# Kernel optimization log

Measured on AMD Instinct MI355X. Metric: run time of the kernel, lower is better.

The kernel has to match this reference:

```python
import jax, jax.numpy as jnp
import numpy as np


def _ln(x, g, b, eps=1e-5):
    m = jnp.mean(x, axis=-1, keepdims=True)
    v = jnp.var(x, axis=-1, keepdims=True)
    return (x - m) * jax.lax.rsqrt(v + eps) * g + b


def setup_inputs() -> dict:
    key = jax.random.key(0)
    ks = jax.random.split(key, 24)
    B, Cin, Cout, Rout, N1, N2 = 8, 256, 512, 256, 4096, 1024
    s = 0.02
    f32 = jnp.float32
    return {
        "l1": jax.random.normal(ks[0], (B, Cin, N1), f32),
        "xyz1": jax.random.normal(ks[1], (B, 3, N1), f32),
        "l2": jax.random.normal(ks[2], (B, Cout, N2), f32),
        "xyz2": jax.random.normal(ks[3], (B, 3, N2), f32),
        # im_choose 1x1 convs (no bias)
        "q1_w": jax.random.normal(ks[4], (Cout, Cin), f32) * s,
        "k1_w": jax.random.normal(ks[5], (Cout, Cin), f32) * s,
        # mlp: Linear(Cin,Cin) -> LN(Cin) -> ReLU -> Linear(Cin,Cout)
        "mlp_w1": jax.random.normal(ks[6], (Cin, Cin), f32) * s,
        "mlp_b1": jnp.zeros((Cin,), f32),
        "mlp_g1": jnp.ones((Cin,), f32),
        "mlp_be1": jnp.zeros((Cin,), f32),
        "mlp_w2": jax.random.normal(ks[7], (Cout, Cin), f32) * s,
        "mlp_b2": jnp.zeros((Cout,), f32),
        # slefAttention 1x1 convs (no bias); pos1 conv is unused in forward
        "qw": jax.random.normal(ks[8], (Cout, Cout), f32) * s,
        "kw": jax.random.normal(ks[9], (Cout, Cout), f32) * s,
        "vw": jax.random.normal(ks[10], (Cout, Cout), f32) * s,
        "posw": jax.random.normal(ks[11], (Cout, 3), f32) * s,
        # IMFF.norm LayerNorm(Cout)
        "norm_g": jnp.ones((Cout,), f32),
        "norm_b": jnp.zeros((Cout,), f32),
        # mlp1: Linear(Cout,Cout) -> LN(Cout) -> ReLU -> Linear(Cout,Rout)
        "m1_w1": jax.random.normal(ks[12], (Cout, Cout), f32) * s,
        "m1_b1": jnp.zeros((Cout,), f32),
        "m1_g": jnp.ones((Cout,), f32),
        "m1_be": jnp.zeros((Cout,), f32),
        "m1_w2": jax.random.normal(ks[13], (Rout, Cout), f32) * s,
        "m1_b2": jnp.zeros((Rout,), f32),
    }


def reference(l1, xyz1, l2, xyz2, q1_w, k1_w, mlp_w1, mlp_b1, mlp_g1, mlp_be1,
              mlp_w2, mlp_b2, qw, kw, vw, posw, norm_g, norm_b,
              m1_w1, m1_b1, m1_g, m1_be, m1_w2, m1_b2):
    Cout = q1_w.shape[0]
    top_k = l2.shape[2]
    scale = jnp.sqrt(jnp.float32(Cout))

    # ---- im_choose: top-k selection of source points via attention row 0 ----
    q1 = jnp.einsum('oc,bcn->bon', q1_w, l1)          # [B,Cout,N1]
    k1 = jnp.einsum('oc,bcn->bon', k1_w, l1)          # [B,Cout,N1]
    e1 = jnp.einsum('bcn,bcm->bnm', q1, k1) / scale   # [B,N1,N1]
    att1 = jax.nn.softmax(e1, axis=-1)
    att_se = att1[:, 0, :]                            # [B,N1]
    _, idx = jax.lax.top_k(att_se, top_k)             # [B,K]
    l1_sel = jnp.take_along_axis(l1, idx[:, None, :], axis=-1)    # [B,Cin,K]
    p1_sel = jnp.take_along_axis(xyz1, idx[:, None, :], axis=-1)  # [B,3,K]

    # ---- mlp on gathered features ----
    h = jnp.swapaxes(l1_sel, 1, 2)                    # [B,K,Cin]
    h = jax.nn.relu(_ln(h @ mlp_w1.T + mlp_b1, mlp_g1, mlp_be1))
    h = h @ mlp_w2.T + mlp_b2                         # [B,K,Cout]
    x2 = jnp.swapaxes(h, 1, 2)                        # [B,Cout,K]

    # ---- slefAttention (cross): x1=l2/xyz2 queries, x2/p1_sel keys+values ----
    pos_q = jnp.einsum('oc,bcn->bon', posw, xyz2)     # [B,Cout,N2]
    pos_k = jnp.einsum('oc,bcn->bon', posw, p1_sel)   # [B,Cout,K]
    q = jnp.einsum('oc,bcn->bon', qw, l2 + pos_q)
    k = jnp.einsum('oc,bcn->bon', kw, x2 + pos_k)
    v = jnp.einsum('oc,bcn->bon', vw, x2)
    e = jnp.einsum('bcn,bcm->bnm', q, k) / scale      # [B,N2,K]
    att = jax.nn.softmax(e, axis=-1)
    o = jnp.einsum('bnm,bcm->bcn', att, v) + l2       # [B,Cout,N2]
    o = jnp.swapaxes(o, 1, 2)                         # [B,N2,Cout]

    # ---- norm + leaky_relu + mlp1 head ----
    o = jax.nn.leaky_relu(_ln(o, norm_g, norm_b), 0.01)
    o = jax.nn.relu(_ln(o @ m1_w1.T + m1_b1, m1_g, m1_be))
    o = o @ m1_w2.T + m1_b2                           # [B,N2,Rout]
    return jnp.swapaxes(o, 1, 2)                      # [B,Rout,N2]
```

## Files before the change

### kernel.cpp

```cpp
#include <hip/hip_runtime.h>
#include <math.h>


typedef __attribute__((ext_vector_type(8))) short short8x;
typedef __attribute__((ext_vector_type(4))) float f32x4;

__device__ __forceinline__ unsigned short f2b(float f) {
  unsigned int u = __float_as_uint(f);
  unsigned int r = u + 0x7FFFu + ((u >> 16) & 1u);
  return (unsigned short)(r >> 16);
}
__device__ __forceinline__ float b2f(unsigned short h) {
  return __uint_as_float(((unsigned int)h) << 16);
}

__device__ __forceinline__ void cp16(const unsigned short* g, unsigned short* l) {
  __builtin_amdgcn_global_load_lds(
      (const __attribute__((address_space(1))) void*)g,
      (__attribute__((address_space(3))) void*)l, 16, 0, 0);
}

__global__ void __launch_bounds__(256) sel_qw_kernel(
    const float* __restrict__ l1, const float* __restrict__ q1w,
    const float* __restrict__ k1w, float* __restrict__ wvec) {
  const int b = blockIdx.x;
  const int t = threadIdx.x;
  __shared__ float col[256];
  __shared__ float q1v[512];
  col[t] = l1[(long)b * 256 * 4096 + (long)t * 4096];
  __syncthreads();
  for (int o = t; o < 512; o += 256) {
    float s = 0.f;
    const float* row = q1w + (long)o * 256;
    for (int c = 0; c < 256; ++c) s += row[c] * col[c];
    q1v[o] = s;
  }
  __syncthreads();
  float s = 0.f;
  for (int o = 0; o < 512; ++o) s += k1w[(long)o * 256 + t] * q1v[o];
  wvec[b * 256 + t] = s;
}

__global__ void __launch_bounds__(256) sel_scores_kernel(
    const float* __restrict__ l1, const float* __restrict__ wvec,
    float* __restrict__ scores) {
  const int b = blockIdx.y;
  const int m = blockIdx.x * 256 + threadIdx.x;
  __shared__ float w[256];
  w[threadIdx.x] = wvec[b * 256 + threadIdx.x];
  __syncthreads();
  const float* base = l1 + (long)b * 256 * 4096 + m;
  float s = 0.f;
  for (int c = 0; c < 256; ++c) s += w[c] * base[(long)c * 4096];
  scores[b * 4096 + m] = s;
}

__global__ void __launch_bounds__(256) topk_select_kernel(
    const float* __restrict__ scores, int* __restrict__ idx_out) {
  const int b = blockIdx.x;
  const int t = threadIdx.x;
  __shared__ unsigned int keys[4096];
  __shared__ unsigned int hist[256];
  __shared__ unsigned int sc_prefix, sc_krem;
  __shared__ int s_bin;
  __shared__ unsigned int partial_gt[256], partial_eq[256];

  for (int m = t; m < 4096; m += 256) {
    unsigned int u = __float_as_uint(scores[b * 4096 + m]);
    u ^= (u & 0x80000000u) ? 0xFFFFFFFFu : 0x80000000u;
    keys[m] = u;
  }
  if (t == 0) { sc_prefix = 0u; sc_krem = 1024u; }
  __syncthreads();

  unsigned int prefmask = 0u;
  for (int shift = 24; shift >= 0; shift -= 8) {
    hist[t] = 0u;
    if (t == 0) s_bin = 0;
    __syncthreads();
    const unsigned int prefix = sc_prefix;
    for (int m = t; m < 4096; m += 256) {
      unsigned int key = keys[m];
      if ((key & prefmask) == prefix) atomicAdd(&hist[(key >> shift) & 255u], 1u);
    }
    __syncthreads();
    for (int off = 1; off < 256; off <<= 1) {
      unsigned int v = hist[t] + ((t + off < 256) ? hist[t + off] : 0u);
      __syncthreads();
      hist[t] = v;
      __syncthreads();
    }
    const unsigned int krem = sc_krem;
    if (hist[t] >= krem) atomicMax(&s_bin, t);
    __syncthreads();
    if (t == 0) {
      const int bin = s_bin;
      sc_krem = krem - ((bin < 255) ? hist[bin + 1] : 0u);
      sc_prefix = prefix | ((unsigned int)bin << shift);
    }
    prefmask |= (0xFFu << shift);
    __syncthreads();
  }
  const unsigned int cutoff = sc_prefix;
  const unsigned int need = sc_krem;

  unsigned int gt = 0u, eq = 0u;
  const int base = t * 16;
  for (int i = 0; i < 16; ++i) {
    unsigned int key = keys[base + i];
    gt += (key > cutoff);
    eq += (key == cutoff);
  }
  partial_gt[t] = gt;
  partial_eq[t] = eq;
  __syncthreads();
  for (int off = 1; off < 256; off <<= 1) {
    unsigned int g = partial_gt[t] + ((t >= off) ? partial_gt[t - off] : 0u);
    unsigned int e2 = partial_eq[t] + ((t >= off) ? partial_eq[t - off] : 0u);
    __syncthreads();
    partial_gt[t] = g;
    partial_eq[t] = e2;
    __syncthreads();
  }
  const unsigned int pref_gt = partial_gt[t] - gt;
  const unsigned int pref_eq = partial_eq[t] - eq;
  unsigned int pos = pref_gt + ((pref_eq < need) ? pref_eq : need);
  unsigned int eqr = pref_eq;
  for (int i = 0; i < 16; ++i) {
    unsigned int key = keys[base + i];
    bool sel = (key > cutoff);
    if (key == cutoff) sel = sel || (eqr++ < need);
    if (sel) idx_out[b * 1024 + (pos++)] = base + i;
  }
}

__global__ void __launch_bounds__(256) gather_sel_kernel(
    const float* __restrict__ l1, const float* __restrict__ xyz1,
    const int* __restrict__ idx, unsigned short* __restrict__ l1selT,
    float* __restrict__ p1selT) {
  const int b = blockIdx.z;
  const int j = blockIdx.x * 64 + (threadIdx.x & 63);
  const int cz = blockIdx.y;
  const int cg = threadIdx.x >> 6;
  const int ix = idx[b * 1024 + j];
  const float* src = l1 + (long)b * 256 * 4096 + ix;
  unsigned short* dst = l1selT + ((long)b * 1024 + j) * 256;
#pragma unroll
  for (int it = 0; it < 8; ++it) {
    const int c = cz * 128 + it * 16 + cg * 4;
    const float x0 = src[(long)(c + 0) * 4096];
    const float x1 = src[(long)(c + 1) * 4096];
    const float x2 = src[(long)(c + 2) * 4096];
    const float x3 = src[(long)(c + 3) * 4096];
    ushort4 o;
    o.x = f2b(x0); o.y = f2b(x1); o.z = f2b(x2); o.w = f2b(x3);
    *(ushort4*)&dst[c] = o;
  }
  if (cz == 0 && cg == 0) {
    float* dp = p1selT + ((long)b * 1024 + j) * 3;
#pragma unroll
    for (int d = 0; d < 3; ++d) dp[d] = xyz1[((long)b * 3 + d) * 4096 + ix];
  }
}

__global__ void __launch_bounds__(256) conv_weights_kernel(
    const float* w0, const float* w1, const float* w2, const float* w3,
    const float* w4, const float* w5, const float* w6,
    unsigned short* d0, unsigned short* d1, unsigned short* d2,
    unsigned short* d3, unsigned short* d4, unsigned short* d5,
    unsigned short* d6) {
  const float* src;
  unsigned short* dst;
  int n;
  switch (blockIdx.y) {
    case 0: src = w0; dst = d0; n = 65536; break;
    case 1: src = w1; dst = d1; n = 131072; break;
    case 2: src = w2; dst = d2; n = 262144; break;
    case 3: src = w3; dst = d3; n = 262144; break;
    case 4: src = w4; dst = d4; n = 262144; break;
    case 5: src = w5; dst = d5; n = 262144; break;
    default: src = w6; dst = d6; n = 131072; break;
  }
  const int i = (blockIdx.x * 256 + threadIdx.x) * 4;
  if (i < n) {
    const float4 v = *(const float4*)(src + i);
    ushort4 o;
    o.x = f2b(v.x); o.y = f2b(v.y); o.z = f2b(v.z); o.w = f2b(v.w);
    *(ushort4*)(dst + i) = o;
  }
}

__global__ void __launch_bounds__(256) transpose_posq_kernel(
    const float* __restrict__ l2, const float* __restrict__ xyz2,
    const float* __restrict__ posw, unsigned short* __restrict__ qinT,
    float* __restrict__ l2T) {
  const int b = blockIdx.z;
  const int n0 = blockIdx.x * 64, c0 = blockIdx.y * 64;
  const int tx = threadIdx.x, ty = threadIdx.y;
  __shared__ float tile[64][65];
  __shared__ float sx[3][64];
  const float* l2b = l2 + (long)b * 512 * 1024;
  for (int r = 0; r < 16; ++r) {
    const int c = ty * 16 + r;
    tile[c][tx] = l2b[(long)(c0 + c) * 1024 + n0 + tx];
  }
  if (ty < 3) sx[ty][tx] = xyz2[((long)b * 3 + ty) * 1024 + n0 + tx];
  __syncthreads();
  const int c = c0 + tx;
  const float p0 = posw[c * 3], p1 = posw[c * 3 + 1], p2 = posw[c * 3 + 2];
  for (int r = 0; r < 16; ++r) {
    const int nl = ty * 16 + r;
    const float val = tile[tx][nl];
    const long o = ((long)b * 1024 + n0 + nl) * 512 + c;
    l2T[o] = val;
    qinT[o] = f2b(val + p0 * sx[0][nl] + p1 * sx[1][nl] + p2 * sx[2][nl]);
  }
}

__global__ void __launch_bounds__(128) kin_kernel(
    const unsigned short* __restrict__ x2T, const float* __restrict__ p1selT,
    const float* __restrict__ posw, unsigned short* __restrict__ kinT) {
  const long row = blockIdx.x;
  const int t = threadIdx.x;
  const float q0 = p1selT[row * 3], q1 = p1selT[row * 3 + 1], q2 = p1selT[row * 3 + 2];
  const int c = t * 4;
  const ushort4 xv = *(const ushort4*)&x2T[row * 512 + c];
  ushort4 o;
  o.x = f2b(b2f(xv.x) + posw[(c + 0) * 3] * q0 + posw[(c + 0) * 3 + 1] * q1 + posw[(c + 0) * 3 + 2] * q2);
  o.y = f2b(b2f(xv.y) + posw[(c + 1) * 3] * q0 + posw[(c + 1) * 3 + 1] * q1 + posw[(c + 1) * 3 + 2] * q2);
  o.z = f2b(b2f(xv.z) + posw[(c + 2) * 3] * q0 + posw[(c + 2) * 3 + 1] * q1 + posw[(c + 2) * 3 + 2] * q2);
  o.w = f2b(b2f(xv.w) + posw[(c + 3) * 3] * q0 + posw[(c + 3) * 3 + 1] * q1 + posw[(c + 3) * 3 + 2] * q2);
  *(ushort4*)&kinT[row * 512 + c] = o;
}

template <bool BIAS_COL, bool BIAS_ROW, bool RES, bool OUT_BF16>
__global__ void __launch_bounds__(256) gemm_bf16(
    const unsigned short* __restrict__ A, long sA, int ldA,
    const unsigned short* __restrict__ Bt, long sB, int ldB, long sB8,
    void* __restrict__ Yv, long sY, int ldY,
    const float* __restrict__ bias, const float* __restrict__ res, long sR,
    int K, float alpha) {
  __shared__ __align__(16) unsigned short ldsA[2][128 * 32];
  __shared__ __align__(16) unsigned short ldsB[2][128 * 32];
  const int tid = threadIdx.x;
  const int lane = tid & 63;
  const int wv = tid >> 6;
  const int wm = wv >> 1, wn = wv & 1;
  const int n0 = blockIdx.x * 128, m0 = blockIdx.y * 128, b = blockIdx.z;
  A += (long)b * sA;
  Bt += (long)(b & 7) * sB + (long)(b >> 3) * sB8;
  const int lane15 = lane & 15, q = lane >> 4;

  const int srow0 = wv * 32 + (lane >> 2);
  const int srow1 = srow0 + 16;
  const int ks0 = ((lane & 3) ^ ((srow0 >> 1) & 3)) << 3;
  const int ks1 = ((lane & 3) ^ ((srow1 >> 1) & 3)) << 3;
  const unsigned short* gA0 = A + (long)(m0 + srow0) * ldA + ks0;
  const unsigned short* gA1 = A + (long)(m0 + srow1) * ldA + ks1;
  const unsigned short* gB0 = Bt + (long)(n0 + srow0) * ldB + ks0;
  const unsigned short* gB1 = Bt + (long)(n0 + srow1) * ldB + ks1;
  unsigned short* lA0[2] = {&ldsA[0][(wv * 32) * 32], &ldsA[1][(wv * 32) * 32]};
  unsigned short* lA1[2] = {&ldsA[0][(wv * 32 + 16) * 32], &ldsA[1][(wv * 32 + 16) * 32]};
  unsigned short* lB0[2] = {&ldsB[0][(wv * 32) * 32], &ldsB[1][(wv * 32) * 32]};
  unsigned short* lB1[2] = {&ldsB[0][(wv * 32 + 16) * 32], &ldsB[1][(wv * 32 + 16) * 32]};

  cp16(gA0, lA0[0]); cp16(gA1, lA1[0]);
  cp16(gB0, lB0[0]); cp16(gB1, lB1[0]);

  f32x4 acc[4][4] = {};
  int cur = 0;
  for (int k0 = 0; k0 < K; k0 += 32) {
    __syncthreads();
    if (k0 + 32 < K) {
      const int nk = k0 + 32;
      cp16(gA0 + nk, lA0[cur ^ 1]); cp16(gA1 + nk, lA1[cur ^ 1]);
      cp16(gB0 + nk, lB0[cur ^ 1]); cp16(gB1 + nk, lB1[cur ^ 1]);
    }
    short8x af[4], bfr[4];
#pragma unroll
    for (int i = 0; i < 4; ++i) {
      const int m = wm * 64 + i * 16 + lane15;
      af[i] = *(const short8x*)&ldsA[cur][m * 32 + ((q ^ ((m >> 1) & 3)) << 3)];
      const int n = wn * 64 + i * 16 + lane15;
      bfr[i] = *(const short8x*)&ldsB[cur][n * 32 + ((q ^ ((n >> 1) & 3)) << 3)];
    }
#pragma unroll
    for (int i = 0; i < 4; ++i)
#pragma unroll
      for (int j = 0; j < 4; ++j)
        acc[i][j] = __builtin_amdgcn_mfma_f32_16x16x32_bf16(af[i], bfr[j], acc[i][j], 0, 0, 0);
    cur ^= 1;
  }

  float* Yf = (float*)Yv + (OUT_BF16 ? 0 : (long)b * sY);
  unsigned short* Yh = (unsigned short*)Yv + (OUT_BF16 ? (long)b * sY : 0);
  if (RES) res += (long)b * sR;
#pragma unroll
  for (int i = 0; i < 4; ++i) {
#pragma unroll
    for (int j = 0; j < 4; ++j) {
      const int n_g = n0 + wn * 64 + j * 16 + lane15;
      const float bc = BIAS_COL ? bias[n_g] : 0.f;
#pragma unroll
      for (int r = 0; r < 4; ++r) {
        const int m_g = m0 + wm * 64 + i * 16 + q * 4 + r;
        float y = acc[i][j][r] * alpha + bc;
        if (BIAS_ROW) y += bias[m_g];
        const long off = (long)m_g * ldY + n_g;
        if (RES) y += res[off];
        if (OUT_BF16) Yh[off] = f2b(y);
        else Yf[off] = y;
      }
    }
  }
}

template <int C>
__global__ void __launch_bounds__(256) row_ln_kernel(
    const float* __restrict__ X, unsigned short* __restrict__ Y,
    const float* __restrict__ g, const float* __restrict__ be, float slope) {
  const int lane = threadIdx.x & 63;
  const long row = (long)blockIdx.x * 4 + (threadIdx.x >> 6);
  const float* xr = X + row * C;
  constexpr int V = C / 256;
  float4 v[V];
  float s = 0.f, sq = 0.f;
#pragma unroll
  for (int u = 0; u < V; ++u) {
    v[u] = ((const float4*)xr)[lane * V + u];
    s += v[u].x + v[u].y + v[u].z + v[u].w;
    sq += v[u].x * v[u].x + v[u].y * v[u].y + v[u].z * v[u].z + v[u].w * v[u].w;
  }
#pragma unroll
  for (int off = 32; off > 0; off >>= 1) {
    s += __shfl_xor(s, off);
    sq += __shfl_xor(sq, off);
  }
  const float mean = s / (float)C;
  const float var = sq / (float)C - mean * mean;
  const float rstd = rsqrtf(var + 1e-5f);
  unsigned short* yr = Y + row * C;
#pragma unroll
  for (int u = 0; u < V; ++u) {
    const int c = (lane * V + u) * 4;
    const float4 gv = ((const float4*)g)[lane * V + u];
    const float4 bv = ((const float4*)be)[lane * V + u];
    float y0 = (v[u].x - mean) * rstd * gv.x + bv.x;
    float y1 = (v[u].y - mean) * rstd * gv.y + bv.y;
    float y2 = (v[u].z - mean) * rstd * gv.z + bv.z;
    float y3 = (v[u].w - mean) * rstd * gv.w + bv.w;
    y0 = y0 > 0.f ? y0 : slope * y0;
    y1 = y1 > 0.f ? y1 : slope * y1;
    y2 = y2 > 0.f ? y2 : slope * y2;
    y3 = y3 > 0.f ? y3 : slope * y3;
    ushort4 o;
    o.x = f2b(y0); o.y = f2b(y1); o.z = f2b(y2); o.w = f2b(y3);
    *(ushort4*)&yr[c] = o;
  }
}

__global__ void __launch_bounds__(256) softmax_bf16_kernel(
    const float* __restrict__ E, unsigned short* __restrict__ att) {
  const long row = blockIdx.x;
  const int t = threadIdx.x;
  float4 v = ((const float4*)(E + row * 1024))[t];
  float m = fmaxf(fmaxf(v.x, v.y), fmaxf(v.z, v.w));
  __shared__ float sm[256];
  sm[t] = m;
  __syncthreads();
  for (int s = 128; s > 0; s >>= 1) {
    if (t < s) sm[t] = fmaxf(sm[t], sm[t + s]);
    __syncthreads();
  }
  m = sm[0];
  __syncthreads();
  v.x = expf(v.x - m); v.y = expf(v.y - m);
  v.z = expf(v.z - m); v.w = expf(v.w - m);
  sm[t] = v.x + v.y + v.z + v.w;
  __syncthreads();
  for (int s = 128; s > 0; s >>= 1) {
    if (t < s) sm[t] += sm[t + s];
    __syncthreads();
  }
  const float inv = 1.f / sm[0];
  ushort4 o;
  o.x = f2b(v.x * inv); o.y = f2b(v.y * inv);
  o.z = f2b(v.z * inv); o.w = f2b(v.w * inv);
  ((ushort4*)(att + row * 1024))[t] = o;
}

extern "C" void kernel_launch(void* const* d_in, const int* in_sizes, int n_in,
                              void* d_out, int out_size, void* d_ws,
                              size_t ws_size, hipStream_t stream) {
  const float* l1 = (const float*)d_in[0];
  const float* xyz1 = (const float*)d_in[1];
  const float* l2 = (const float*)d_in[2];
  const float* xyz2 = (const float*)d_in[3];
  const float* q1w = (const float*)d_in[4];
  const float* k1w = (const float*)d_in[5];
  const float* mlp_w1 = (const float*)d_in[6];
  const float* mlp_b1 = (const float*)d_in[7];
  const float* mlp_g1 = (const float*)d_in[8];
  const float* mlp_be1 = (const float*)d_in[9];
  const float* mlp_w2 = (const float*)d_in[10];
  const float* mlp_b2 = (const float*)d_in[11];
  const float* qw = (const float*)d_in[12];
  const float* kw = (const float*)d_in[13];
  const float* vw = (const float*)d_in[14];
  const float* posw = (const float*)d_in[15];
  const float* norm_g = (const float*)d_in[16];
  const float* norm_b = (const float*)d_in[17];
  const float* m1_w1 = (const float*)d_in[18];
  const float* m1_b1 = (const float*)d_in[19];
  const float* m1_g = (const float*)d_in[20];
  const float* m1_be = (const float*)d_in[21];
  const float* m1_w2 = (const float*)d_in[22];
  const float* m1_b2 = (const float*)d_in[23];

  char* ws = (char*)d_ws;
  const long MiB = 1048576;
  unsigned short* wb_mlp_w1 = (unsigned short*)(ws + 0);
  unsigned short* wb_mlp_w2 = (unsigned short*)(ws + 131072);
  unsigned short* wb_qw = (unsigned short*)(ws + 393216);
  unsigned short* wb_kw = (unsigned short*)(ws + 917504);
  unsigned short* wb_vw = (unsigned short*)(ws + 1441792);
  unsigned short* wb_m1w1 = (unsigned short*)(ws + 1966080);
  unsigned short* wb_m1w2 = (unsigned short*)(ws + 2490368);
  float* scores = (float*)(ws + 2752512);
  float* wvec = (float*)(ws + 2883584);
  int* idxb = (int*)(ws + 2891776);
  float* p1selT = (float*)(ws + 2924544);
  float* e = (float*)(ws + 4 * MiB);
  unsigned short* l1selT = (unsigned short*)(ws + 4 * MiB);
  float* h1raw = (float*)(ws + 8 * MiB);
  unsigned short* h1T = (unsigned short*)(ws + 16 * MiB);
  unsigned short* qinT = (unsigned short*)(ws + 20 * MiB);
  unsigned short* kinT = (unsigned short*)(ws + 28 * MiB);
  float* l2T = (float*)(ws + 36 * MiB);
  unsigned short* x2T = (unsigned short*)(ws + 52 * MiB);
  unsigned short* g2T = (unsigned short*)(ws + 52 * MiB);
  unsigned short* qT = (unsigned short*)(ws + 60 * MiB);
  unsigned short* kT = (unsigned short*)(ws + 68 * MiB);
  float* oraw = (float*)(ws + 60 * MiB);
  unsigned short* vbf = (unsigned short*)(ws + 76 * MiB);
  unsigned short* att = (unsigned short*)(ws + 84 * MiB);
  float* g1raw = (float*)(ws + 84 * MiB);
  unsigned short* o1T = (unsigned short*)(ws + 100 * MiB);
  float* outp = (float*)d_out;

  const float inv_scale = 1.0f / sqrtf(512.0f);
  const long T256 = 1024L * 256, T512 = 1024L * 512, T1024 = 1024L * 1024;

  conv_weights_kernel<<<dim3(256, 7), 256, 0, stream>>>(
      mlp_w1, mlp_w2, qw, kw, vw, m1_w1, m1_w2,
      wb_mlp_w1, wb_mlp_w2, wb_qw, wb_kw, wb_vw, wb_m1w1, wb_m1w2);
  sel_qw_kernel<<<8, 256, 0, stream>>>(l1, q1w, k1w, wvec);
  sel_scores_kernel<<<dim3(16, 8), 256, 0, stream>>>(l1, wvec, scores);
  topk_select_kernel<<<8, 256, 0, stream>>>(scores, idxb);
  gather_sel_kernel<<<dim3(16, 2, 8), 256, 0, stream>>>(l1, xyz1, idxb, l1selT, p1selT);

  gemm_bf16<true, false, false, false><<<dim3(2, 8, 8), 256, 0, stream>>>(
      l1selT, T256, 256, wb_mlp_w1, 0, 256, 0, h1raw, T256, 256, mlp_b1, nullptr, 0, 256, 1.0f);
  row_ln_kernel<256><<<2048, 256, 0, stream>>>(h1raw, h1T, mlp_g1, mlp_be1, 0.0f);
  gemm_bf16<true, false, false, true><<<dim3(4, 8, 8), 256, 0, stream>>>(
      h1T, T256, 256, wb_mlp_w2, 0, 256, 0, x2T, T512, 512, mlp_b2, nullptr, 0, 256, 1.0f);

  transpose_posq_kernel<<<dim3(16, 8, 8), dim3(64, 4), 0, stream>>>(
      l2, xyz2, posw, qinT, l2T);
  kin_kernel<<<8192, 128, 0, stream>>>(x2T, p1selT, posw, kinT);

  gemm_bf16<false, false, false, true><<<dim3(4, 8, 16), 256, 0, stream>>>(
      qinT, T512, 512, wb_qw, 0, 512, 262144, qT, T512, 512, nullptr, nullptr, 0, 512, 1.0f);
  gemm_bf16<false, false, false, true><<<dim3(8, 4, 8), 256, 0, stream>>>(
      wb_vw, 0, 512, x2T, T512, 512, 0, vbf, T512, 1024, nullptr, nullptr, 0, 512, 1.0f);

  gemm_bf16<false, false, false, false><<<dim3(8, 8, 8), 256, 0, stream>>>(
      qT, T512, 512, kT, T512, 512, 0, e, T1024, 1024, nullptr, nullptr, 0, 512, inv_scale);
  softmax_bf16_kernel<<<8192, 256, 0, stream>>>(e, att);
  gemm_bf16<false, false, true, false><<<dim3(4, 8, 8), 256, 0, stream>>>(
      att, T1024, 1024, vbf, T512, 1024, 0, oraw, T512, 512, nullptr, l2T, T512, 1024, 1.0f);

  row_ln_kernel<512><<<2048, 256, 0, stream>>>(oraw, o1T, norm_g, norm_b, 0.01f);
  gemm_bf16<true, false, false, false><<<dim3(4, 8, 8), 256, 0, stream>>>(
      o1T, T512, 512, wb_m1w1, 0, 512, 0, g1raw, T512, 512, m1_b1, nullptr, 0, 512, 1.0f);
  row_ln_kernel<512><<<2048, 256, 0, stream>>>(g1raw, g2T, m1_g, m1_be, 0.0f);
  gemm_bf16<false, true, false, false><<<dim3(8, 2, 8), 256, 0, stream>>>(
      wb_m1w2, 0, 512, g2T, T512, 512, 0, outp, 256L * 1024, 1024, m1_b2, nullptr, 0, 512, 1.0f);
}
```

Before: 355.4 us.

## Fuse LayerNorm and softmax into GEMM prologues and epilogues using atomic row statistics

```diff
diff --git a/kernel.cpp b/kernel.cpp
--- a/kernel.cpp
+++ b/kernel.cpp
@@ -20,25 +20,53 @@
       (__attribute__((address_space(3))) void*)l, 16, 0, 0);
 }
 
-__global__ void __launch_bounds__(256) sel_qw_kernel(
+__global__ void __launch_bounds__(256) prep_kernel(
+    const float* w0, const float* w1, const float* w2, const float* w3,
+    const float* w4, const float* w5, const float* w6,
+    unsigned short* d0, unsigned short* d1, unsigned short* d2,
+    unsigned short* d3, unsigned short* d4, unsigned short* d5,
+    unsigned short* d6,
     const float* __restrict__ l1, const float* __restrict__ q1w,
     const float* __restrict__ k1w, float* __restrict__ wvec) {
-  const int b = blockIdx.x;
-  const int t = threadIdx.x;
-  __shared__ float col[256];
-  __shared__ float q1v[512];
-  col[t] = l1[(long)b * 256 * 4096 + (long)t * 4096];
-  __syncthreads();
-  for (int o = t; o < 512; o += 256) {
+  if (blockIdx.y == 7) {
+    if (blockIdx.x >= 8) return;
+    const int b = blockIdx.x;
+    const int t = threadIdx.x;
+    __shared__ float col[256];
+    __shared__ float q1v[512];
+    col[t] = l1[(long)b * 256 * 4096 + (long)t * 4096];
+    __syncthreads();
+    for (int o = t; o < 512; o += 256) {
+      float s = 0.f;
+      const float* row = q1w + (long)o * 256;
+      for (int c = 0; c < 256; ++c) s += row[c] * col[c];
+      q1v[o] = s;
+    }
+    __syncthreads();
     float s = 0.f;
-    const float* row = q1w + (long)o * 256;
-    for (int c = 0; c < 256; ++c) s += row[c] * col[c];
-    q1v[o] = s;
-  }
-  __syncthreads();
-  float s = 0.f;
-  for (int o = 0; o < 512; ++o) s += k1w[(long)o * 256 + t] * q1v[o];
-  wvec[b * 256 + t] = s;
+    for (int o = 0; o < 512; ++o) s += k1w[(long)o * 256 + t] * q1v[o];
+    wvec[b * 256 + t] = s;
+    return;
+  }
+  const float* src;
+  unsigned short* dst;
+  int n;
+  switch (blockIdx.y) {
+    case 0: src = w0; dst = d0; n = 65536; break;
+    case 1: src = w1; dst = d1; n = 131072; break;
+    case 2: src = w2; dst = d2; n = 262144; break;
+    case 3: src = w3; dst = d3; n = 262144; break;
+    case 4: src = w4; dst = d4; n = 262144; break;
+    case 5: src = w5; dst = d5; n = 262144; break;
+    default: src = w6; dst = d6; n = 131072; break;
+  }
+  const int i = (blockIdx.x * 256 + threadIdx.x) * 4;
+  if (i < n) {
+    const float4 v = *(const float4*)(src + i);
+    ushort4 o;
+    o.x = f2b(v.x); o.y = f2b(v.y); o.z = f2b(v.z); o.w = f2b(v.w);
+    *(ushort4*)(dst + i) = o;
+  }
 }
 
 __global__ void __launch_bounds__(256) sel_scores_kernel(
@@ -160,33 +188,6 @@
     float* dp = p1selT + ((long)b * 1024 + j) * 3;
 #pragma unroll
     for (int d = 0; d < 3; ++d) dp[d] = xyz1[((long)b * 3 + d) * 4096 + ix];
-  }
-}
-
-__global__ void __launch_bounds__(256) conv_weights_kernel(
-    const float* w0, const float* w1, const float* w2, const float* w3,
-    const float* w4, const float* w5, const float* w6,
-    unsigned short* d0, unsigned short* d1, unsigned short* d2,
-    unsigned short* d3, unsigned short* d4, unsigned short* d5,
-    unsigned short* d6) {
-  const float* src;
-  unsigned short* dst;
-  int n;
-  switch (blockIdx.y) {
-    case 0: src = w0; dst = d0; n = 65536; break;
-    case 1: src = w1; dst = d1; n = 131072; break;
-    case 2: src = w2; dst = d2; n = 262144; break;
-    case 3: src = w3; dst = d3; n = 262144; break;
-    case 4: src = w4; dst = d4; n = 262144; break;
-    case 5: src = w5; dst = d5; n = 262144; break;
-    default: src = w6; dst = d6; n = 131072; break;
-  }
-  const int i = (blockIdx.x * 256 + threadIdx.x) * 4;
-  if (i < n) {
-    const float4 v = *(const float4*)(src + i);
-    ushort4 o;
-    o.x = f2b(v.x); o.y = f2b(v.y); o.z = f2b(v.z); o.w = f2b(v.w);
-    *(ushort4*)(dst + i) = o;
   }
 }
 
@@ -233,13 +234,17 @@
   *(ushort4*)&kinT[row * 512 + c] = o;
 }
 
-template <bool BIAS_COL, bool BIAS_ROW, bool RES, bool OUT_BF16>
-__global__ void __launch_bounds__(256) gemm_bf16(
+template <int TRA, int TRB, bool BCOL, bool BROW, bool RES, int EPI>
+__global__ void __launch_bounds__(256) gemm_u(
     const unsigned short* __restrict__ A, long sA, int ldA,
     const unsigned short* __restrict__ Bt, long sB, int ldB, long sB8,
     void* __restrict__ Yv, long sY, int ldY,
-    const float* __restrict__ bias, const float* __restrict__ res, long sR,
-    int K, float alpha) {
+    const float* __restrict__ bias,
+    const float* __restrict__ res, long sR,
+    int K, float alpha,
+    const float* __restrict__ ts1, const float* __restrict__ ts2,
+    const float* __restrict__ tg, const float* __restrict__ tb, float tslope,
+    float* __restrict__ os1, float* __restrict__ os2) {
   __shared__ __align__(16) unsigned short ldsA[2][128 * 32];
   __shared__ __align__(16) unsigned short ldsB[2][128 * 32];
   const int tid = threadIdx.x;
@@ -264,17 +269,74 @@
   unsigned short* lB0[2] = {&ldsB[0][(wv * 32) * 32], &ldsB[1][(wv * 32) * 32]};
   unsigned short* lB1[2] = {&ldsB[0][(wv * 32 + 16) * 32], &ldsB[1][(wv * 32 + 16) * 32]};
 
-  cp16(gA0, lA0[0]); cp16(gA1, lA1[0]);
-  cp16(gB0, lB0[0]); cp16(gB1, lB1[0]);
+  constexpr bool TR = (TRA + TRB) != 0;
+  const int trow = tid & 127, thalf = tid >> 7;
+  float t_mu = 0.f, t_rs = 0.f;
+  const unsigned short* tsrc = nullptr;
+  int toff0 = 0, toff1 = 0;
+  if constexpr (TR) {
+    const int row0 = (TRA ? m0 : n0) + trow;
+    const int ridx = (b & 7) * 1024 + row0;
+    const float Cf = (float)K;
+    const float s1v = ts1[ridx], s2v = ts2[ridx];
+    t_mu = s1v / Cf;
+    t_rs = rsqrtf(s2v / Cf - t_mu * t_mu + 1e-5f);
+    tsrc = (TRA ? A + (long)row0 * ldA : Bt + (long)row0 * ldB) + thalf * 16;
+    const int sw = (trow >> 1) & 3;
+    toff0 = trow * 32 + ((((thalf * 2) ^ sw)) << 3);
+    toff1 = trow * 32 + ((((thalf * 2 + 1) ^ sw)) << 3);
+  }
+
+  auto t_apply = [&](int kk, short8x r0, short8x r1, int buf) {
+    union { short8x v; unsigned short u[8]; } a0, a1, w0, w1;
+    a0.v = r0; a1.v = r1;
+    const float4* gp = (const float4*)(tg + kk + thalf * 16);
+    const float4* bp = (const float4*)(tb + kk + thalf * 16);
+    const float4 g0 = gp[0], g1 = gp[1], g2 = gp[2], g3 = gp[3];
+    const float4 e0 = bp[0], e1 = bp[1], e2 = bp[2], e3 = bp[3];
+    const float gg[16] = {g0.x, g0.y, g0.z, g0.w, g1.x, g1.y, g1.z, g1.w,
+                          g2.x, g2.y, g2.z, g2.w, g3.x, g3.y, g3.z, g3.w};
+    const float ee[16] = {e0.x, e0.y, e0.z, e0.w, e1.x, e1.y, e1.z, e1.w,
+                          e2.x, e2.y, e2.z, e2.w, e3.x, e3.y, e3.z, e3.w};
+#pragma unroll
+    for (int c = 0; c < 8; ++c) {
+      float y = (b2f(a0.u[c]) - t_mu) * t_rs * gg[c] + ee[c];
+      y = y > 0.f ? y : tslope * y;
+      w0.u[c] = f2b(y);
+    }
+#pragma unroll
+    for (int c = 0; c < 8; ++c) {
+      float y = (b2f(a1.u[c]) - t_mu) * t_rs * gg[8 + c] + ee[8 + c];
+      y = y > 0.f ? y : tslope * y;
+      w1.u[c] = f2b(y);
+    }
+    unsigned short* base = TRA ? &ldsA[buf][0] : &ldsB[buf][0];
+    *(short8x*)&base[toff0] = w0.v;
+    *(short8x*)&base[toff1] = w1.v;
+  };
+
+  short8x tr0, tr1;
+  if constexpr (TR) {
+    tr0 = *(const short8x*)(tsrc + 0);
+    tr1 = *(const short8x*)(tsrc + 8);
+  }
+  if constexpr (!TRA) { cp16(gA0, lA0[0]); cp16(gA1, lA1[0]); }
+  if constexpr (!TRB) { cp16(gB0, lB0[0]); cp16(gB1, lB1[0]); }
+  if constexpr (TR) t_apply(0, tr0, tr1, 0);
 
   f32x4 acc[4][4] = {};
   int cur = 0;
   for (int k0 = 0; k0 < K; k0 += 32) {
     __syncthreads();
-    if (k0 + 32 < K) {
+    const bool nxt = (k0 + 32 < K);
+    if (nxt) {
       const int nk = k0 + 32;
-      cp16(gA0 + nk, lA0[cur ^ 1]); cp16(gA1 + nk, lA1[cur ^ 1]);
-      cp16(gB0 + nk, lB0[cur ^ 1]); cp16(gB1 + nk, lB1[cur ^ 1]);
+      if constexpr (!TRA) { cp16(gA0 + nk, lA0[cur ^ 1]); cp16(gA1 + nk, lA1[cur ^ 1]); }
+      if constexpr (!TRB) { cp16(gB0 + nk, lB0[cur ^ 1]); cp16(gB1 + nk, lB1[cur ^ 1]); }
+      if constexpr (TR) {
+        tr0 = *(const short8x*)(tsrc + nk);
+        tr1 = *(const short8x*)(tsrc + nk + 8);
+      }
     }
     short8x af[4], bfr[4];
 #pragma unroll
@@ -289,104 +351,82 @@
 #pragma unroll
       for (int j = 0; j < 4; ++j)
         acc[i][j] = __builtin_amdgcn_mfma_f32_16x16x32_bf16(af[i], bfr[j], acc[i][j], 0, 0, 0);
+    if (nxt) {
+      if constexpr (TR) t_apply(k0 + 32, tr0, tr1, cur ^ 1);
+    }
     cur ^= 1;
   }
 
-  float* Yf = (float*)Yv + (OUT_BF16 ? 0 : (long)b * sY);
-  unsigned short* Yh = (unsigned short*)Yv + (OUT_BF16 ? (long)b * sY : 0);
-  if (RES) res += (long)b * sR;
+  float* Yf = (float*)Yv;
+  unsigned short* Yh = (unsigned short*)Yv;
+  if constexpr (EPI == 0) Yf += (long)b * sY; else Yh += (long)b * sY;
+  if constexpr (RES) res += (long)b * sR;
+  float inv_[4];
+  float ssum[4][4], ssq[4][4];
+#pragma unroll
+  for (int i = 0; i < 4; ++i)
+#pragma unroll
+    for (int r = 0; r < 4; ++r) { ssum[i][r] = 0.f; ssq[i][r] = 0.f; }
+
 #pragma unroll
   for (int i = 0; i < 4; ++i) {
+    if constexpr (EPI == 4) {
+#pragma unroll
+      for (int r = 0; r < 4; ++r)
+        inv_[r] = 1.f / ts1[(b & 7) * 1024 + m0 + wm * 64 + i * 16 + q * 4 + r];
+    }
 #pragma unroll
     for (int j = 0; j < 4; ++j) {
       const int n_g = n0 + wn * 64 + j * 16 + lane15;
-      const float bc = BIAS_COL ? bias[n_g] : 0.f;
+      const float bc = BCOL ? bias[n_g] : 0.f;
 #pragma unroll
       for (int r = 0; r < 4; ++r) {
         const int m_g = m0 + wm * 64 + i * 16 + q * 4 + r;
-        float y = acc[i][j][r] * alpha + bc;
-        if (BIAS_ROW) y += bias[m_g];
+        float y = acc[i][j][r] * alpha;
+        if constexpr (EPI == 4) y *= inv_[r];
+        if constexpr (BCOL) y += bc;
+        if constexpr (BROW) y += bias[m_g];
+        if constexpr (RES) y += res[(long)m_g * ldY + n_g];
+        if constexpr (EPI == 3) y = __expf(y);
         const long off = (long)m_g * ldY + n_g;
-        if (RES) y += res[off];
-        if (OUT_BF16) Yh[off] = f2b(y);
-        else Yf[off] = y;
+        if constexpr (EPI == 0) Yf[off] = y;
+        else Yh[off] = f2b(y);
+        if constexpr (EPI >= 2) { ssum[i][r] += y; ssq[i][r] += y * y; }
       }
     }
   }
-}
-
-template <int C>
-__global__ void __launch_bounds__(256) row_ln_kernel(
-    const float* __restrict__ X, unsigned short* __restrict__ Y,
-    const float* __restrict__ g, const float* __restrict__ be, float slope) {
-  const int lane = threadIdx.x & 63;
-  const long row = (long)blockIdx.x * 4 + (threadIdx.x >> 6);
-  const float* xr = X + row * C;
-  constexpr int V = C / 256;
-  float4 v[V];
-  float s = 0.f, sq = 0.f;
-#pragma unroll
-  for (int u = 0; u < V; ++u) {
-    v[u] = ((const float4*)xr)[lane * V + u];
-    s += v[u].x + v[u].y + v[u].z + v[u].w;
-    sq += v[u].x * v[u].x + v[u].y * v[u].y + v[u].z * v[u].z + v[u].w * v[u].w;
-  }
-#pragma unroll
-  for (int off = 32; off > 0; off >>= 1) {
-    s += __shfl_xor(s, off);
-    sq += __shfl_xor(sq, off);
-  }
-  const float mean = s / (float)C;
-  const float var = sq / (float)C - mean * mean;
-  const float rstd = rsqrtf(var + 1e-5f);
-  unsigned short* yr = Y + row * C;
-#pragma unroll
-  for (int u = 0; u < V; ++u) {
-    const int c = (lane * V + u) * 4;
-    const float4 gv = ((const float4*)g)[lane * V + u];
-    const float4 bv = ((const float4*)be)[lane * V + u];
-    float y0 = (v[u].x - mean) * rstd * gv.x + bv.x;
-    float y1 = (v[u].y - mean) * rstd * gv.y + bv.y;
-    float y2 = (v[u].z - mean) * rstd * gv.z + bv.z;
-    float y3 = (v[u].w - mean) * rstd * gv.w + bv.w;
-    y0 = y0 > 0.f ? y0 : slope * y0;
-    y1 = y1 > 0.f ? y1 : slope * y1;
-    y2 = y2 > 0.f ? y2 : slope * y2;
-    y3 = y3 > 0.f ? y3 : slope * y3;
-    ushort4 o;
-    o.x = f2b(y0); o.y = f2b(y1); o.z = f2b(y2); o.w = f2b(y3);
-    *(ushort4*)&yr[c] = o;
-  }
-}
-
-__global__ void __launch_bounds__(256) softmax_bf16_kernel(
-    const float* __restrict__ E, unsigned short* __restrict__ att) {
-  const long row = blockIdx.x;
-  const int t = threadIdx.x;
-  float4 v = ((const float4*)(E + row * 1024))[t];
-  float m = fmaxf(fmaxf(v.x, v.y), fmaxf(v.z, v.w));
-  __shared__ float sm[256];
-  sm[t] = m;
-  __syncthreads();
-  for (int s = 128; s > 0; s >>= 1) {
-    if (t < s) sm[t] = fmaxf(sm[t], sm[t + s]);
-    __syncthreads();
-  }
-  m = sm[0];
-  __syncthreads();
-  v.x = expf(v.x - m); v.y = expf(v.y - m);
-  v.z = expf(v.z - m); v.w = expf(v.w - m);
-  sm[t] = v.x + v.y + v.z + v.w;
-  __syncthreads();
-  for (int s = 128; s > 0; s >>= 1) {
-    if (t < s) sm[t] += sm[t + s];
-    __syncthreads();
-  }
-  const float inv = 1.f / sm[0];
-  ushort4 o;
-  o.x = f2b(v.x * inv); o.y = f2b(v.y * inv);
-  o.z = f2b(v.z * inv); o.w = f2b(v.w * inv);
-  ((ushort4*)(att + row * 1024))[t] = o;
+  if constexpr (EPI == 2 || EPI == 4) {
+#pragma unroll
+    for (int i = 0; i < 4; ++i)
+#pragma unroll
+      for (int r = 0; r < 4; ++r) {
+        float s = ssum[i][r], q2 = ssq[i][r];
+        s += __shfl_xor(s, 1); q2 += __shfl_xor(q2, 1);
+        s += __shfl_xor(s, 2); q2 += __shfl_xor(q2, 2);
+        s += __shfl_xor(s, 4); q2 += __shfl_xor(q2, 4);
+        s += __shfl_xor(s, 8); q2 += __shfl_xor(q2, 8);
+        if (lane15 == 0) {
+          const int ridx = (b & 7) * 1024 + m0 + wm * 64 + i * 16 + q * 4 + r;
+          atomicAdd(&os1[ridx], s);
+          atomicAdd(&os2[ridx], q2);
+        }
+      }
+  } else if constexpr (EPI == 3) {
+#pragma unroll
+    for (int i = 0; i < 4; ++i)
+#pragma unroll
+      for (int r = 0; r < 4; ++r) {
+        float s = ssum[i][r];
+        s += __shfl_xor(s, 1);
+        s += __shfl_xor(s, 2);
+        s += __shfl_xor(s, 4);
+        s += __shfl_xor(s, 8);
+        if (lane15 == 0) {
+          const int ridx = (b & 7) * 1024 + m0 + wm * 64 + i * 16 + q * 4 + r;
+          atomicAdd(&os1[ridx], s);
+        }
+      }
+  }
 }
 
 extern "C" void kernel_launch(void* const* d_in, const int* in_sizes, int n_in,
@@ -430,60 +470,68 @@
   float* wvec = (float*)(ws + 2883584);
   int* idxb = (int*)(ws + 2891776);
   float* p1selT = (float*)(ws + 2924544);
-  float* e = (float*)(ws + 4 * MiB);
+  float* rowsum = (float*)(ws + 3407872);
+  float* h1_s1 = (float*)(ws + 3440640);
+  float* h1_s2 = (float*)(ws + 3473408);
+  float* o_s1 = (float*)(ws + 3506176);
+  float* o_s2 = (float*)(ws + 3538944);
+  float* g1_s1 = (float*)(ws + 3571712);
+  float* g1_s2 = (float*)(ws + 3604480);
   unsigned short* l1selT = (unsigned short*)(ws + 4 * MiB);
-  float* h1raw = (float*)(ws + 8 * MiB);
-  unsigned short* h1T = (unsigned short*)(ws + 16 * MiB);
+  unsigned short* h1 = (unsigned short*)(ws + 8 * MiB);
+  unsigned short* x2T = (unsigned short*)(ws + 12 * MiB);
   unsigned short* qinT = (unsigned short*)(ws + 20 * MiB);
   unsigned short* kinT = (unsigned short*)(ws + 28 * MiB);
   float* l2T = (float*)(ws + 36 * MiB);
-  unsigned short* x2T = (unsigned short*)(ws + 52 * MiB);
-  unsigned short* g2T = (unsigned short*)(ws + 52 * MiB);
-  unsigned short* qT = (unsigned short*)(ws + 60 * MiB);
-  unsigned short* kT = (unsigned short*)(ws + 68 * MiB);
-  float* oraw = (float*)(ws + 60 * MiB);
-  unsigned short* vbf = (unsigned short*)(ws + 76 * MiB);
-  unsigned short* att = (unsigned short*)(ws + 84 * MiB);
-  float* g1raw = (float*)(ws + 84 * MiB);
-  unsigned short* o1T = (unsigned short*)(ws + 100 * MiB);
+  unsigned short* qT = (unsigned short*)(ws + 52 * MiB);
+  unsigned short* kT = (unsigned short*)(ws + 60 * MiB);
+  unsigned short* vbf = (unsigned short*)(ws + 68 * MiB);
+  unsigned short* pbuf = (unsigned short*)(ws + 76 * MiB);
+  unsigned short* obuf = (unsigned short*)(ws + 92 * MiB);
+  unsigned short* g1buf = (unsigned short*)(ws + 100 * MiB);
   float* outp = (float*)d_out;
 
   const float inv_scale = 1.0f / sqrtf(512.0f);
   const long T256 = 1024L * 256, T512 = 1024L * 512, T1024 = 1024L * 1024;
 
-  conv_weights_kernel<<<dim3(256, 7), 256, 0, stream>>>(
+  hipMemsetAsync(ws + 3407872, 0, 7 * 32768, stream);
+
+  prep_kernel<<<dim3(256, 8), 256, 0, stream>>>(
       mlp_w1, mlp_w2, qw, kw, vw, m1_w1, m1_w2,
-      wb_mlp_w1, wb_mlp_w2, wb_qw, wb_kw, wb_vw, wb_m1w1, wb_m1w2);
-  sel_qw_kernel<<<8, 256, 0, stream>>>(l1, q1w, k1w, wvec);
+      wb_mlp_w1, wb_mlp_w2, wb_qw, wb_kw, wb_vw, wb_m1w1, wb_m1w2,
+      l1, q1w, k1w, wvec);
   sel_scores_kernel<<<dim3(16, 8), 256, 0, stream>>>(l1, wvec, scores);
   topk_select_kernel<<<8, 256, 0, stream>>>(scores, idxb);
   gather_sel_kernel<<<dim3(16, 2, 8), 256, 0, stream>>>(l1, xyz1, idxb, l1selT, p1selT);
-
-  gemm_bf16<true, false, false, false><<<dim3(2, 8, 8), 256, 0, stream>>>(
-      l1selT, T256, 256, wb_mlp_w1, 0, 256, 0, h1raw, T256, 256, mlp_b1, nullptr, 0, 256, 1.0f);
-  row_ln_kernel<256><<<2048, 256, 0, stream>>>(h1raw, h1T, mlp_g1, mlp_be1, 0.0f);
-  gemm_bf16<true, false, false, true><<<dim3(4, 8, 8), 256, 0, stream>>>(
-      h1T, T256, 256, wb_mlp_w2, 0, 256, 0, x2T, T512, 512, mlp_b2, nullptr, 0, 256, 1.0f);
-
   transpose_posq_kernel<<<dim3(16, 8, 8), dim3(64, 4), 0, stream>>>(
       l2, xyz2, posw, qinT, l2T);
+
+  gemm_u<0, 0, true, false, false, 2><<<dim3(2, 8, 8), 256, 0, stream>>>(
+      l1selT, T256, 256, wb_mlp_w1, 0, 256, 0, h1, T256, 256, mlp_b1,
+      nullptr, 0, 256, 1.0f, nullptr, nullptr, nullptr, nullptr, 0.f, h1_s1, h1_s2);
+  gemm_u<1, 0, true, false, false, 1><<<dim3(4, 8, 8), 256, 0, stream>>>(
+      h1, T256, 256, wb_mlp_w2, 0, 256, 0, x2T, T512, 512, mlp_b2,
+      nullptr, 0, 256, 1.0f, h1_s1, h1_s2, mlp_g1, mlp_be1, 0.f, nullptr, nullptr);
+
   kin_kernel<<<8192, 128, 0, stream>>>(x2T, p1selT, posw, kinT);
 
-  gemm_bf16<false, false, false, true><<<dim3(4, 8, 16), 256, 0, stream>>>(
-      qinT, T512, 512, wb_qw, 0, 512, 262144, qT, T512, 512, nullptr, nullptr, 0, 512, 1.0f);
-  gemm_bf16<false, false, false, true><<<dim3(8, 4, 8), 256, 0, stream>>>(
-      wb_vw, 0, 512, x2T, T512, 512, 0, vbf, T512, 1024, nullptr, nullptr, 0, 512, 1.0f);
-
-  gemm_bf16<false, false, false, false><<<dim3(8, 8, 8), 256, 0, stream>>>(
-      qT, T512, 512, kT, T512, 512, 0, e, T1024, 1024, nullptr, nullptr, 0, 512, inv_scale);
-  softmax_bf16_kernel<<<8192, 256, 0, stream>>>(e, att);
-  gemm_bf16<false, false, true, false><<<dim3(4, 8, 8), 256, 0, stream>>>(
-      att, T1024, 1024, vbf, T512, 1024, 0, oraw, T512, 512, nullptr, l2T, T512, 1024, 1.0f);
-
-  row_ln_kernel<512><<<2048, 256, 0, stream>>>(oraw, o1T, norm_g, norm_b, 0.01f);
-  gemm_bf16<true, false, false, false><<<dim3(4, 8, 8), 256, 0, stream>>>(
-      o1T, T512, 512, wb_m1w1, 0, 512, 0, g1raw, T512, 512, m1_b1, nullptr, 0, 512, 1.0f);
-  row_ln_kernel<512><<<2048, 256, 0, stream>>>(g1raw, g2T, m1_g, m1_be, 0.0f);
-  gemm_bf16<false, true, false, false><<<dim3(8, 2, 8), 256, 0, stream>>>(
-      wb_m1w2, 0, 512, g2T, T512, 512, 0, outp, 256L * 1024, 1024, m1_b2, nullptr, 0, 512, 1.0f);
-}
+  gemm_u<0, 0, false, false, false, 1><<<dim3(4, 8, 16), 256, 0, stream>>>(
+      qinT, T512, 512, wb_qw, 0, 512, 262144, qT, T512, 512, nullptr,
+      nullptr, 0, 512, 1.0f, nullptr, nullptr, nullptr, nullptr, 0.f, nullptr, nullptr);
+  gemm_u<0, 0, false, false, false, 1><<<dim3(8, 4, 8), 256, 0, stream>>>(
+      wb_vw, 0, 512, x2T, T512, 512, 0, vbf, T512, 1024, nullptr,
+      nullptr, 0, 512, 1.0f, nullptr, nullptr, nullptr, nullptr, 0.f, nullptr, nullptr);
+
+  gemm_u<0, 0, false, false, false, 3><<<dim3(8, 8, 8), 256, 0, stream>>>(
+      qT, T512, 512, kT, T512, 512, 0, pbuf, T1024, 1024, nullptr,
+      nullptr, 0, 512, inv_scale, nullptr, nullptr, nullptr, nullptr, 0.f, rowsum, nullptr);
+  gemm_u<0, 0, false, false, true, 4><<<dim3(4, 8, 8), 256, 0, stream>>>(
+      pbuf, T1024, 1024, vbf, T512, 1024, 0, obuf, T512, 512, nullptr,
+      l2T, T512, 1024, 1.0f, rowsum, nullptr, nullptr, nullptr, 0.f, o_s1, o_s2);
+  gemm_u<1, 0, true, false, false, 2><<<dim3(4, 8, 8), 256, 0, stream>>>(
+      obuf, T512, 512, wb_m1w1, 0, 512, 0, g1buf, T512, 512, m1_b1,
+      nullptr, 0, 512, 1.0f, o_s1, o_s2, norm_g, norm_b, 0.01f, g1_s1, g1_s2);
+  gemm_u<0, 1, false, true, false, 0><<<dim3(8, 2, 8), 256, 0, stream>>>(
+      wb_m1w2, 0, 512, g1buf, T512, 512, 0, outp, 256L * 1024, 1024, m1_b2,
+      nullptr, 0, 512, 1.0f, g1_s1, g1_s2, m1_g, m1_be, 0.f, nullptr, nullptr);
+}
```

Measured after the change: 371.9 us. +4.6%, slower.
